# Performance work log

Hardware: AMD Instinct MI355X
Metric: run time of the kernel (lower is better)

Reference implementation:

```python
import jax, jax.numpy as jnp
import numpy as np
from jax import lax

MARGIN = 0.3
BIGF = 1e9


def _pairwise_dist(x):
    # dist[i,j] = ||x_i - x_j||, clamped at 1e-12 before sqrt (as in torch code)
    sq = jnp.sum(x * x, axis=1)
    d = sq[:, None] + sq[None, :] - 2.0 * (x @ x.T)
    return jnp.sqrt(jnp.clip(d, 1e-12))


def _hard_mining(dist, targets):
    is_pos = targets[:, None] == targets[None, :]
    ap = jnp.where(is_pos, dist, jnp.asarray(-BIGF, dist.dtype))
    an = jnp.where(is_pos, jnp.asarray(BIGF, dist.dtype), dist)
    dist_ap = jnp.max(ap, axis=1)
    p_inds = jnp.argmax(ap, axis=1)
    dist_an = jnp.min(an, axis=1)
    n_inds = jnp.argmin(an, axis=1)
    return dist_ap, dist_an, p_inds, n_inds


def _batch_euclidean(x, y):
    # x: [N,m,d], y: [N,n,d] -> [N,m,n]
    xx = jnp.sum(x * x, axis=-1)[:, :, None]
    yy = jnp.sum(y * y, axis=-1)[:, None, :]
    d = xx + yy - 2.0 * jnp.einsum('nmd,nkd->nmk', x, y)
    return jnp.sqrt(jnp.clip(d, 1e-12))


def _shortest_dist(dmat):
    # DTW-style shortest path over [m,n] grid, batched over N: dp[i,j] = d[i,j] + min(dp[i-1,j], dp[i,j-1])
    N, m, n = dmat.shape
    big = jnp.asarray(BIGF, dmat.dtype)
    init_row = jnp.full((N, n), big, dmat.dtype).at[:, 0].set(0.0)  # virtual row -1: only (0,0) reachable

    def row_step(prev_row, drow):  # prev_row,drow: [N,n]
        def col_step(left, un):  # left: [N]
            up, d = un
            cur = d + jnp.minimum(up, left)
            return cur, cur
        _, cols = lax.scan(col_step, jnp.full((N,), big, dmat.dtype), (prev_row.T, drow.T))
        return cols.T, None

    last_row, _ = lax.scan(row_step, init_row, jnp.moveaxis(dmat, 1, 0))
    return last_row[:, -1]


def _batch_local_dist(x, y):
    d = _batch_euclidean(x, y)
    d = jnp.tanh(d * 0.5)  # == (exp(d)-1)/(exp(d)+1), numerically safe
    return _shortest_dist(d)


def _margin_ranking(dist_an, dist_ap, margin):
    # MarginRankingLoss with y=1: mean(relu(margin - (dist_an - dist_ap)))
    return jnp.mean(jnp.maximum(0.0, margin + dist_ap - dist_an))


def setup_inputs() -> dict:
    key = jax.random.key(0)
    k1, k2 = jax.random.split(key)
    N, D = 512, 2048
    LD, PARTS = 128, 8
    K = 4  # instances per identity (PK sampling)
    inputs = jax.random.normal(k1, (N, D), dtype=jnp.float32)
    local_features = jax.random.normal(k2, (N, LD, PARTS), dtype=jnp.float32)
    targets = jnp.arange(N, dtype=jnp.int64) // K
    return {"inputs": inputs, "targets": targets, "local_features": local_features}


def reference(inputs, targets, local_features):
    dist = _pairwise_dist(inputs)
    dist_ap, dist_an, p_inds, n_inds = _hard_mining(dist, targets)
    global_loss = _margin_ranking(dist_an, dist_ap, MARGIN)
    lf = jnp.transpose(local_features, (0, 2, 1))  # [N, parts, local_dim]
    local_ap = _batch_local_dist(lf, lf[p_inds])
    local_an = _batch_local_dist(lf, lf[n_inds])
    local_loss = _margin_ranking(local_an, local_ap, MARGIN)
    return (global_loss, local_loss)
```

## Files before the change

### kernel.cpp

```cpp
#include <hip/hip_runtime.h>
#include <math.h>

#define MARGIN 0.3f
#define BIGF 1e9f
#define NN 512
#define DD 2048
#define LDIM 128
#define PARTS 8

typedef __attribute__((ext_vector_type(8))) __bf16 bf16x8;
typedef __attribute__((ext_vector_type(4))) float f32x4;

__global__ __launch_bounds__(256, 2) void k_gram(
    const float* __restrict__ X, float* __restrict__ Gp,
    float* __restrict__ ndiag, float* gsum, float* lsum, unsigned* counter)
{
    __shared__ __bf16 A[2][4096], B[2][4096];

    int bid = blockIdx.x;
    int tj = bid & 7, ti = (bid >> 3) & 7, ks = bid >> 6;
    int t = threadIdx.x;
    int w = t >> 6, lane = t & 63;
    int wr = w >> 1, wc = w & 1;

    if (bid == 0 && t == 0) { *gsum = 0.0f; *lsum = 0.0f; *counter = 0u; }

    int m = t >> 7;
    int r = (t >> 1) & 63;
    int kst = t & 1;
    int grow = (m ? tj : ti) * 64 + r;
    const float4* gp4 = (const float4*)(X + (size_t)grow * DD + ks * 256 + kst * 32);
    int ebase = kst * 2048 + (r >> 4) * 512 + (r & 15) * 8;

    float4 cur[8];
#pragma unroll
    for (int q = 0; q < 8; q++) cur[q] = gp4[q];

    f32x4 acc00 = {0.f, 0.f, 0.f, 0.f};
    f32x4 acc01 = {0.f, 0.f, 0.f, 0.f};
    f32x4 acc10 = {0.f, 0.f, 0.f, 0.f};
    f32x4 acc11 = {0.f, 0.f, 0.f, 0.f};

    {
        __bf16* hb = (m ? B[0] : A[0]) + ebase;
#pragma unroll
        for (int jg = 0; jg < 4; jg++) {
            float fe[8] = {cur[2 * jg].x, cur[2 * jg].y, cur[2 * jg].z, cur[2 * jg].w,
                           cur[2 * jg + 1].x, cur[2 * jg + 1].y, cur[2 * jg + 1].z, cur[2 * jg + 1].w};
            bf16x8 h;
#pragma unroll
            for (int e = 0; e < 8; e++) h[e] = (__bf16)fe[e];
            *(bf16x8*)(hb + jg * 128) = h;
        }
    }

#pragma unroll
    for (int it = 0; it < 4; ++it) {
        __syncthreads();
        if (it < 3) {
            const float4* np = gp4 + (it + 1) * 16;
#pragma unroll
            for (int q = 0; q < 8; q++) cur[q] = np[q];
        }
        int buf = it & 1;
#pragma unroll
        for (int kstep = 0; kstep < 2; kstep++) {
            const bf16x8* fA = (const bf16x8*)&A[buf][kstep * 2048 + wr * 1024];
            const bf16x8* fB = (const bf16x8*)&B[buf][kstep * 2048 + wc * 1024];
            bf16x8 ah0 = fA[lane], ah1 = fA[lane + 64];
            bf16x8 bh0 = fB[lane], bh1 = fB[lane + 64];
            acc00 = __builtin_amdgcn_mfma_f32_16x16x32_bf16(ah0, bh0, acc00, 0, 0, 0);
            acc01 = __builtin_amdgcn_mfma_f32_16x16x32_bf16(ah0, bh1, acc01, 0, 0, 0);
            acc10 = __builtin_amdgcn_mfma_f32_16x16x32_bf16(ah1, bh0, acc10, 0, 0, 0);
            acc11 = __builtin_amdgcn_mfma_f32_16x16x32_bf16(ah1, bh1, acc11, 0, 0, 0);
        }
        if (it < 3) {
            int nb = (it + 1) & 1;
            __bf16* hb = (m ? B[nb] : A[nb]) + ebase;
#pragma unroll
            for (int jg = 0; jg < 4; jg++) {
                float fe[8] = {cur[2 * jg].x, cur[2 * jg].y, cur[2 * jg].z, cur[2 * jg].w,
                               cur[2 * jg + 1].x, cur[2 * jg + 1].y, cur[2 * jg + 1].z, cur[2 * jg + 1].w};
                bf16x8 h;
#pragma unroll
                for (int e = 0; e < 8; e++) h[e] = (__bf16)fe[e];
                *(bf16x8*)(hb + jg * 128) = h;
            }
        }
    }

    int rbase = ti * 64 + wr * 32 + ((lane >> 4) << 2);
    int cbase = tj * 64 + wc * 32 + (lane & 15);
    float* gb = Gp + (size_t)ks * NN * NN;
    f32x4 accs[2][2] = {{acc00, acc01}, {acc10, acc11}};
#pragma unroll
    for (int g = 0; g < 2; g++)
#pragma unroll
        for (int h = 0; h < 2; h++)
#pragma unroll
            for (int rr = 0; rr < 4; rr++)
                gb[(size_t)(rbase + g * 16 + rr) * NN + cbase + h * 16] = accs[g][h][rr];

    if (ti == tj && wr == wc && ((lane >> 4) == ((lane & 15) >> 2))) {
        int rr = lane & 3;
        int row0 = rbase + rr;
        ndiag[ks * NN + row0]      = acc00[rr];
        ndiag[ks * NN + row0 + 16] = acc11[rr];
    }
}

__global__ __launch_bounds__(256) void k_mine_local(
    const float* __restrict__ Gp, const float* __restrict__ ndiag,
    const int* __restrict__ tg, const float* __restrict__ LF,
    float* gsum, float* lsum, unsigned* counter, float* __restrict__ out)
{
    __shared__ float sdiag[NN];
    __shared__ float s_apv[4]; __shared__ int s_api[4];
    __shared__ float s_anv[4]; __shared__ int s_ani[4];
    __shared__ int sh_pn[2];
    __shared__ float A2[LDIM * PARTS];
    __shared__ float B2[2][LDIM * PARTS];
    __shared__ float dtm[2][64];
    __shared__ float res[2];

    int i = blockIdx.x;
    int t = threadIdx.x;

    float d0 = 0.f, d1 = 0.f;
#pragma unroll
    for (int ks = 0; ks < 8; ks++) {
        d0 += ndiag[ks * NN + t];
        d1 += ndiag[ks * NN + t + 256];
    }
    sdiag[t] = d0;
    sdiag[t + 256] = d1;
    __syncthreads();

    float ni = sdiag[i];
    int tgt_i = tg[i];

    float apv = -BIGF; int api = 0x7fffffff;
    float anv =  BIGF; int ani = 0x7fffffff;

#pragma unroll
    for (int jj = 0; jj < 2; jj++) {
        int j = t + jj * 256;
        float g = 0.f;
#pragma unroll
        for (int ks = 0; ks < 8; ks++)
            g += Gp[(size_t)ks * NN * NN + (size_t)i * NN + j];
        float nj = (jj == 0) ? d0 : d1;
        float dd = ni + nj - 2.0f * g;
        float dist = sqrtf(fmaxf(dd, 1e-12f));
        bool pos = (tg[j] == tgt_i);
        float a = pos ? dist : -BIGF;
        if (a > apv || (a == apv && j < api)) { apv = a; api = j; }
        float b = pos ? BIGF : dist;
        if (b < anv || (b == anv && j < ani)) { anv = b; ani = j; }
    }
    for (int off = 32; off > 0; off >>= 1) {
        float av = __shfl_down(apv, off); int ai = __shfl_down(api, off);
        if (av > apv || (av == apv && ai < api)) { apv = av; api = ai; }
        float nv = __shfl_down(anv, off); int nid = __shfl_down(ani, off);
        if (nv < anv || (nv == anv && nid < ani)) { anv = nv; ani = nid; }
    }
    int lane = t & 63, wid = t >> 6;
    if (lane == 0) { s_apv[wid] = apv; s_api[wid] = api;
                     s_anv[wid] = anv; s_ani[wid] = ani; }
    __syncthreads();
    if (t == 0) {
        apv = s_apv[0]; api = s_api[0]; anv = s_anv[0]; ani = s_ani[0];
        for (int wv = 1; wv < 4; wv++) {
            float av = s_apv[wv]; int ai = s_api[wv];
            if (av > apv || (av == apv && ai < api)) { apv = av; api = ai; }
            float nv = s_anv[wv]; int nid = s_ani[wv];
            if (nv < anv || (nv == anv && nid < ani)) { anv = nv; ani = nid; }
        }
        sh_pn[0] = api;
        sh_pn[1] = ani;
        atomicAdd(gsum, fmaxf(0.0f, MARGIN + apv - anv));
    }
    __syncthreads();

    int w = t >> 6;
    ((float4*)A2)[t] = ((const float4*)(LF + (size_t)i * LDIM * PARTS))[t];
    if (w < 2) {
        int ind = sh_pn[w];
        const float4* B4 = (const float4*)(LF + (size_t)ind * LDIM * PARTS);
        float4* Bw = (float4*)B2[w];
        Bw[lane]       = B4[lane];
        Bw[lane + 64]  = B4[lane + 64];
        Bw[lane + 128] = B4[lane + 128];
        Bw[lane + 192] = B4[lane + 192];
    }
    __syncthreads();

    if (w < 2) {
        int p = lane >> 3, q = lane & 7;
        float acc = 0.0f;
        const float* Bw = B2[w];
        for (int d = 0; d < LDIM; d++) {
            float diff = A2[d * PARTS + p] - Bw[d * PARTS + q];
            acc = fmaf(diff, diff, acc);
        }
        float dist = sqrtf(fmaxf(acc, 1e-12f));
        dtm[w][p * 8 + q] = tanhf(0.5f * dist);
    }
    __syncthreads();

    if ((t == 0) || (t == 64)) {
        const float* dm = dtm[w];
        float dp[8];
        dp[0] = dm[0];
        for (int j = 1; j < 8; j++) dp[j] = dp[j - 1] + dm[j];
        for (int rr = 1; rr < 8; rr++) {
            dp[0] += dm[rr * 8];
            for (int j = 1; j < 8; j++)
                dp[j] = dm[rr * 8 + j] + fminf(dp[j], dp[j - 1]);
        }
        res[w] = dp[7];
    }
    __syncthreads();

    if (t == 0) {
        float l = fmaxf(0.0f, MARGIN + res[0] - res[1]);
        atomicAdd(lsum, l);
        __threadfence();
        unsigned old = atomicAdd(counter, 1u);
        if (old == (NN - 1)) {
            __threadfence();
            float ls = atomicAdd(lsum, 0.0f);
            float gs = atomicAdd(gsum, 0.0f);
            out[0] = gs * (1.0f / NN);
            out[1] = ls * (1.0f / NN);
        }
    }
}

extern "C" void kernel_launch(void* const* d_in, const int* in_sizes, int n_in,
                              void* d_out, int out_size, void* d_ws, size_t ws_size,
                              hipStream_t stream)
{
    const float* X  = (const float*)d_in[0];
    const int*   tg = (const int*)d_in[1];
    const float* LF = (const float*)d_in[2];
    float* out = (float*)d_out;

    char* ws = (char*)d_ws;
    float*    Gp      = (float*)ws;
    float*    ndiag   = (float*)(ws + (8u << 20));
    float*    gsum    = (float*)(ws + (8u << 20) + 16384);
    float*    lsum    = (float*)(ws + (8u << 20) + 16388);
    unsigned* counter = (unsigned*)(ws + (8u << 20) + 16392);

    k_gram<<<512, 256, 0, stream>>>(X, Gp, ndiag, gsum, lsum, counter);
    k_mine_local<<<512, 256, 0, stream>>>(Gp, ndiag, tg, LF, gsum, lsum, counter, out);
}
```

Measured before the change: 94.97 us.

## Fuse gram and mining kernels with a software grid barrier

Merges the Gram-matrix kernel and the hard-mining/local-distance kernel into one launch of 512 blocks, separated by an atomic-counter grid barrier with sleep polling. Counters are zeroed with a hipMemsetAsync before the launch. The aim is to remove the second kernel launch and the gap between the two kernels. The cost is extra shared-memory usage, which can lower occupancy. The barrier also risks deadlock if all 512 blocks cannot be co-resident, and it adds a memset node to the stream.

```diff
diff --git a/kernel.cpp b/kernel.cpp
--- a/kernel.cpp
+++ b/kernel.cpp
@@ -11,19 +11,27 @@
 typedef __attribute__((ext_vector_type(8))) __bf16 bf16x8;
 typedef __attribute__((ext_vector_type(4))) float f32x4;
 
-__global__ __launch_bounds__(256, 2) void k_gram(
-    const float* __restrict__ X, float* __restrict__ Gp,
-    float* __restrict__ ndiag, float* gsum, float* lsum, unsigned* counter)
+__global__ __launch_bounds__(256, 2) void k_fused(
+    const float* __restrict__ X, const int* __restrict__ tg,
+    const float* __restrict__ LF, float* __restrict__ Gp,
+    float* __restrict__ ndiag, float* gsum, float* lsum,
+    unsigned* ticket, unsigned* bar, float* __restrict__ out)
 {
     __shared__ __bf16 A[2][4096], B[2][4096];
+    __shared__ float sdiag[NN];
+    __shared__ float s_apv[4]; __shared__ int s_api[4];
+    __shared__ float s_anv[4]; __shared__ int s_ani[4];
+    __shared__ int sh_pn[2];
+    __shared__ float A2[LDIM * PARTS];
+    __shared__ float B2[2][LDIM * PARTS];
+    __shared__ float dtm[2][64];
+    __shared__ float res[2];
 
     int bid = blockIdx.x;
     int tj = bid & 7, ti = (bid >> 3) & 7, ks = bid >> 6;
     int t = threadIdx.x;
     int w = t >> 6, lane = t & 63;
     int wr = w >> 1, wc = w & 1;
-
-    if (bid == 0 && t == 0) { *gsum = 0.0f; *lsum = 0.0f; *counter = 0u; }
 
     int m = t >> 7;
     int r = (t >> 1) & 63;
@@ -107,30 +115,25 @@
         ndiag[ks * NN + row0]      = acc00[rr];
         ndiag[ks * NN + row0 + 16] = acc11[rr];
     }
-}
-
-__global__ __launch_bounds__(256) void k_mine_local(
-    const float* __restrict__ Gp, const float* __restrict__ ndiag,
-    const int* __restrict__ tg, const float* __restrict__ LF,
-    float* gsum, float* lsum, unsigned* counter, float* __restrict__ out)
-{
-    __shared__ float sdiag[NN];
-    __shared__ float s_apv[4]; __shared__ int s_api[4];
-    __shared__ float s_anv[4]; __shared__ int s_ani[4];
-    __shared__ int sh_pn[2];
-    __shared__ float A2[LDIM * PARTS];
-    __shared__ float B2[2][LDIM * PARTS];
-    __shared__ float dtm[2][64];
-    __shared__ float res[2];
-
-    int i = blockIdx.x;
-    int t = threadIdx.x;
+
+    __syncthreads();
+    if (t == 0) {
+        __threadfence();
+        __hip_atomic_fetch_add(bar, 1u, __ATOMIC_RELAXED, __HIP_MEMORY_SCOPE_AGENT);
+        while (__hip_atomic_load(bar, __ATOMIC_RELAXED, __HIP_MEMORY_SCOPE_AGENT)
+               < (unsigned)NN)
+            __builtin_amdgcn_s_sleep(8);
+        (void)__hip_atomic_load(bar, __ATOMIC_ACQUIRE, __HIP_MEMORY_SCOPE_AGENT);
+    }
+    __syncthreads();
+
+    int i = bid;
 
     float d0 = 0.f, d1 = 0.f;
 #pragma unroll
-    for (int ks = 0; ks < 8; ks++) {
-        d0 += ndiag[ks * NN + t];
-        d1 += ndiag[ks * NN + t + 256];
+    for (int kk = 0; kk < 8; kk++) {
+        d0 += ndiag[kk * NN + t];
+        d1 += ndiag[kk * NN + t + 256];
     }
     sdiag[t] = d0;
     sdiag[t + 256] = d1;
@@ -147,8 +150,8 @@
         int j = t + jj * 256;
         float g = 0.f;
 #pragma unroll
-        for (int ks = 0; ks < 8; ks++)
-            g += Gp[(size_t)ks * NN * NN + (size_t)i * NN + j];
+        for (int kk = 0; kk < 8; kk++)
+            g += Gp[(size_t)kk * NN * NN + (size_t)i * NN + j];
         float nj = (jj == 0) ? d0 : d1;
         float dd = ni + nj - 2.0f * g;
         float dist = sqrtf(fmaxf(dd, 1e-12f));
@@ -164,9 +167,8 @@
         float nv = __shfl_down(anv, off); int nid = __shfl_down(ani, off);
         if (nv < anv || (nv == anv && nid < ani)) { anv = nv; ani = nid; }
     }
-    int lane = t & 63, wid = t >> 6;
-    if (lane == 0) { s_apv[wid] = apv; s_api[wid] = api;
-                     s_anv[wid] = anv; s_ani[wid] = ani; }
+    if (lane == 0) { s_apv[w] = apv; s_api[w] = api;
+                     s_anv[w] = anv; s_ani[w] = ani; }
     __syncthreads();
     if (t == 0) {
         apv = s_apv[0]; api = s_api[0]; anv = s_anv[0]; ani = s_ani[0];
@@ -182,7 +184,6 @@
     }
     __syncthreads();
 
-    int w = t >> 6;
     ((float4*)A2)[t] = ((const float4*)(LF + (size_t)i * LDIM * PARTS))[t];
     if (w < 2) {
         int ind = sh_pn[w];
@@ -226,7 +227,7 @@
         float l = fmaxf(0.0f, MARGIN + res[0] - res[1]);
         atomicAdd(lsum, l);
         __threadfence();
-        unsigned old = atomicAdd(counter, 1u);
+        unsigned old = atomicAdd(ticket, 1u);
         if (old == (NN - 1)) {
             __threadfence();
             float ls = atomicAdd(lsum, 0.0f);
@@ -249,10 +250,13 @@
     char* ws = (char*)d_ws;
     float*    Gp      = (float*)ws;
     float*    ndiag   = (float*)(ws + (8u << 20));
-    float*    gsum    = (float*)(ws + (8u << 20) + 16384);
-    float*    lsum    = (float*)(ws + (8u << 20) + 16388);
-    unsigned* counter = (unsigned*)(ws + (8u << 20) + 16392);
-
-    k_gram<<<512, 256, 0, stream>>>(X, Gp, ndiag, gsum, lsum, counter);
-    k_mine_local<<<512, 256, 0, stream>>>(Gp, ndiag, tg, LF, gsum, lsum, counter, out);
+    char*     ctr     = ws + (8u << 20) + 16384;
+    float*    gsum    = (float*)(ctr + 0);
+    float*    lsum    = (float*)(ctr + 4);
+    unsigned* ticket  = (unsigned*)(ctr + 8);
+    unsigned* bar     = (unsigned*)(ctr + 12);
+
+    hipMemsetAsync(ctr, 0, 16, stream);
+    k_fused<<<NN, 256, 0, stream>>>(X, tg, LF, Gp, ndiag, gsum, lsum,
+                                    ticket, bar, out);
 }
```

Result: slower. 148.4 us (+56.3%).
